# Optimization experiments

Hardware: AMD Instinct MI355X
Metric: run time of the kernel (lower is better)

## Reference

```python
import jax, jax.numpy as jnp
import numpy as np

N_NODES = 1_000_000
N_EDGES = 16_000_000


def _mean_aggregate(x, src, dst, num_nodes):
    # PyG message passing: message x_j = x[src], mean-aggregated at dst.
    msgs = x[src]  # [E, d]
    sums = jax.ops.segment_sum(msgs, dst, num_segments=num_nodes)
    cnt = jax.ops.segment_sum(jnp.ones((src.shape[0],), x.dtype), dst,
                              num_segments=num_nodes)
    return sums / jnp.maximum(cnt, 1.0)[:, None]


def _sage_conv(x, src, dst, W_l, b_l, W_r, num_nodes):
    # PyG SAGEConv (aggr='mean'): out = lin_l(mean_j x_j) + lin_r(x_i)
    agg = _mean_aggregate(x, src, dst, num_nodes)
    return agg @ W_l + b_l + x @ W_r


def setup_inputs() -> dict:
    key = jax.random.key(0)
    ks = jax.random.split(key, 12)
    x = jax.random.normal(ks[0], (N_NODES, 1), dtype=jnp.float32)
    edge_index = jax.random.randint(ks[1], (2, N_EDGES), 0, N_NODES, dtype=jnp.int64)

    def lin(k, din, dout):
        s = 1.0 / np.sqrt(din)
        return jax.random.uniform(k, (din, dout), jnp.float32, -s, s)

    return {
        "x": x, "edge_index": edge_index,
        "W1l": lin(ks[2], 1, 4), "b1": jnp.zeros((4,), jnp.float32), "W1r": lin(ks[3], 1, 4),
        "W2l": lin(ks[4], 4, 4), "b2": jnp.zeros((4,), jnp.float32), "W2r": lin(ks[5], 4, 4),
        "W3l": lin(ks[6], 4, 2), "b3": jnp.zeros((2,), jnp.float32), "W3r": lin(ks[7], 4, 2),
        "Wc": lin(ks[8], 2, 2), "bc": jnp.zeros((2,), jnp.float32),
    }


def reference(x, edge_index, W1l, b1, W1r, W2l, b2, W2r, W3l, b3, W3r, Wc, bc):
    src, dst = edge_index[0], edge_index[1]
    n = x.shape[0]
    h = jax.nn.relu(_sage_conv(x, src, dst, W1l, b1, W1r, n))
    h = jax.nn.relu(_sage_conv(h, src, dst, W2l, b2, W2r, n))
    h = jax.nn.relu(_sage_conv(h, src, dst, W3l, b3, W3r, n))
    out = h @ Wc + bc
    return (out, h)
```

## Files before the change

kernel.cpp:

```cpp
#include <hip/hip_runtime.h>
#include <hip/hip_fp16.h>


#define NBUCK 4096
#define CAP   4608
#define SRCM  0xFFFFFu
#define DEPTH 8

__device__ __forceinline__ ushort4 pack_h4(float4 f)
{
    ushort4 r;
    r.x = __half_as_ushort(__float2half_rn(f.x));
    r.y = __half_as_ushort(__float2half_rn(f.y));
    r.z = __half_as_ushort(__float2half_rn(f.z));
    r.w = __half_as_ushort(__float2half_rn(f.w));
    return r;
}

__device__ __forceinline__ float4 unpack_h4(ushort4 v)
{
    return make_float4(__half2float(__ushort_as_half(v.x)),
                       __half2float(__ushort_as_half(v.y)),
                       __half2float(__ushort_as_half(v.z)),
                       __half2float(__ushort_as_half(v.w)));
}

__global__ __launch_bounds__(256) void init_cursor(unsigned* __restrict__ cursor)
{
    int b = blockIdx.x * blockDim.x + threadIdx.x;
    if (b < NBUCK) cursor[b] = (unsigned)b * CAP;
}

__global__ __launch_bounds__(1024) void scatter_staged(
    const int* __restrict__ ei,
    unsigned* __restrict__ gcur,
    unsigned* __restrict__ bucket,
    long long E, long long chunk)
{
    __shared__ unsigned stage[NBUCK * DEPTH];
    __shared__ unsigned cnt[NBUCK];
    const int t = threadIdx.x;
    const long long beg = (long long)blockIdx.x * chunk;
    const long long end = min(E, beg + chunk);

    for (int i = t; i < NBUCK; i += 1024) cnt[i] = 0;
    __syncthreads();

    for (long long base = beg; base < end; base += 4096) {
        unsigned rec[4], bk[4], pos[4];
        int nv = 0;
        long long i = base + (long long)t * 4;
        if (i + 4 <= end) {
            int4 s4 = *reinterpret_cast<const int4*>(ei + i);
            int4 d4 = *reinterpret_cast<const int4*>(ei + E + i);
            rec[0] = (unsigned)s4.x | (((unsigned)d4.x & 255u) << 20); bk[0] = (unsigned)d4.x >> 8;
            rec[1] = (unsigned)s4.y | (((unsigned)d4.y & 255u) << 20); bk[1] = (unsigned)d4.y >> 8;
            rec[2] = (unsigned)s4.z | (((unsigned)d4.z & 255u) << 20); bk[2] = (unsigned)d4.z >> 8;
            rec[3] = (unsigned)s4.w | (((unsigned)d4.w & 255u) << 20); bk[3] = (unsigned)d4.w >> 8;
            nv = 4;
        } else {
            for (long long j = i; j < end && nv < 4; ++j) {
                unsigned s = (unsigned)ei[j];
                unsigned d = (unsigned)ei[E + j];
                rec[nv] = s | ((d & 255u) << 20);
                bk[nv] = d >> 8;
                ++nv;
            }
        }
        for (int k = 0; k < nv; ++k) pos[k] = atomicAdd(&cnt[bk[k]], 1u);
        __syncthreads();
        for (int k = 0; k < nv; ++k)
            if (pos[k] < DEPTH) stage[bk[k] * DEPTH + pos[k]] = rec[k];
        __syncthreads();
        for (int bb = t; bb < NBUCK; bb += 1024) {
            unsigned c = cnt[bb];
            if (c >= DEPTH) {
                unsigned gb = atomicAdd(&gcur[bb], DEPTH);
                unsigned lim = (unsigned)(bb + 1) * CAP;
#pragma unroll
                for (int k = 0; k < DEPTH; ++k)
                    if (gb + k < lim) bucket[gb + k] = stage[bb * DEPTH + k];
                cnt[bb] = 0;
            }
        }
        __syncthreads();
        for (int k = 0; k < nv; ++k) {
            if (pos[k] >= DEPTH) {
                unsigned p2 = atomicAdd(&cnt[bk[k]], 1u);
                if (p2 < DEPTH) stage[bk[k] * DEPTH + p2] = rec[k];
                else {
                    unsigned gb = atomicAdd(&gcur[bk[k]], 1u);
                    if (gb < (unsigned)(bk[k] + 1) * CAP) bucket[gb] = rec[k];
                }
            }
        }
        __syncthreads();
    }
    for (int bb = t; bb < NBUCK; bb += 1024) {
        unsigned c = min(cnt[bb], (unsigned)DEPTH);
        if (c) {
            unsigned gb = atomicAdd(&gcur[bb], c);
            unsigned lim = (unsigned)(bb + 1) * CAP;
            for (unsigned k = 0; k < c; ++k)
                if (gb + k < lim) bucket[gb + k] = stage[bb * DEPTH + k];
        }
    }
}

template <bool EMIT16>
__global__ __launch_bounds__(256) void sort_l1(
    unsigned* __restrict__ bucket,
    const unsigned* __restrict__ cursor,
    unsigned* __restrict__ meta,
    const float* __restrict__ x,
    const float* __restrict__ W1l, const float* __restrict__ b1,
    const float* __restrict__ W1r,
    float* __restrict__ invout, float4* __restrict__ h1,
    ushort4* __restrict__ h1h, int N)
{
    __shared__ unsigned recA[CAP];
    __shared__ unsigned recB[CAP];
    __shared__ unsigned hist[256], pref[256], curs[256];
    const int t = threadIdx.x;
    const unsigned b = blockIdx.x;
    const unsigned base = b * CAP;
    const unsigned cnt = min(cursor[b] - base, (unsigned)CAP);

    hist[t] = 0;
    __syncthreads();
    for (unsigned i = t; i < cnt; i += 256) {
        unsigned r = bucket[base + i];
        recA[i] = r;
        atomicAdd(&hist[r >> 20], 1u);
    }
    __syncthreads();
    unsigned v = hist[t];
    pref[t] = v;
    __syncthreads();
    for (int off = 1; off < 256; off <<= 1) {
        unsigned u = (t >= off) ? pref[t - off] : 0u;
        __syncthreads();
        pref[t] += u;
        __syncthreads();
    }
    unsigned excl = pref[t] - v;
    curs[t] = excl;
    __syncthreads();
    for (unsigned i = t; i < cnt; i += 256) {
        unsigned r = recA[i];
        unsigned pos = atomicAdd(&curs[r >> 20], 1u);
        recB[pos] = r & SRCM;
    }
    __syncthreads();
    for (unsigned i = t; i < cnt; i += 256)
        bucket[base + i] = recB[i];

    int dst = (int)(b * 256u) + t;
    if (dst >= N) return;
    meta[dst] = excl | (v << 16);

    float sum = 0.0f;
    for (unsigned j = 0; j < v; ++j)
        sum += x[recB[excl + j]];
    float iv = 1.0f / fmaxf((float)v, 1.0f);
    invout[dst] = iv;
    float a = sum * iv;
    float xv = x[dst];
    float4 h;
    h.x = fmaxf(a * W1l[0] + b1[0] + xv * W1r[0], 0.0f);
    h.y = fmaxf(a * W1l[1] + b1[1] + xv * W1r[1], 0.0f);
    h.z = fmaxf(a * W1l[2] + b1[2] + xv * W1r[2], 0.0f);
    h.w = fmaxf(a * W1l[3] + b1[3] + xv * W1r[3], 0.0f);
    h1[dst] = h;
    if (EMIT16) h1h[dst] = pack_h4(h);
}

__device__ __forceinline__ float4 run_sum4(
    const unsigned* srtd, unsigned idx, unsigned c,
    const float4* __restrict__ feat)
{
    float a0 = 0, a1 = 0, a2 = 0, a3 = 0;
    unsigned j = 0;
    for (; j + 4 <= c; j += 4) {
        unsigned s0 = srtd[idx + j + 0];
        unsigned s1 = srtd[idx + j + 1];
        unsigned s2 = srtd[idx + j + 2];
        unsigned s3 = srtd[idx + j + 3];
        float4 f0 = feat[s0];
        float4 f1 = feat[s1];
        float4 f2 = feat[s2];
        float4 f3 = feat[s3];
        a0 += f0.x + f1.x + f2.x + f3.x;
        a1 += f0.y + f1.y + f2.y + f3.y;
        a2 += f0.z + f1.z + f2.z + f3.z;
        a3 += f0.w + f1.w + f2.w + f3.w;
    }
    for (; j < c; ++j) {
        float4 f = feat[srtd[idx + j]];
        a0 += f.x; a1 += f.y; a2 += f.z; a3 += f.w;
    }
    return make_float4(a0, a1, a2, a3);
}

__device__ __forceinline__ float4 run_sum4h(
    const unsigned* srtd, unsigned idx, unsigned c,
    const ushort4* __restrict__ feat)
{
    float a0 = 0, a1 = 0, a2 = 0, a3 = 0;
    unsigned j = 0;
    for (; j + 4 <= c; j += 4) {
        unsigned s0 = srtd[idx + j + 0];
        unsigned s1 = srtd[idx + j + 1];
        unsigned s2 = srtd[idx + j + 2];
        unsigned s3 = srtd[idx + j + 3];
        float4 f0 = unpack_h4(feat[s0]);
        float4 f1 = unpack_h4(feat[s1]);
        float4 f2 = unpack_h4(feat[s2]);
        float4 f3 = unpack_h4(feat[s3]);
        a0 += f0.x + f1.x + f2.x + f3.x;
        a1 += f0.y + f1.y + f2.y + f3.y;
        a2 += f0.z + f1.z + f2.z + f3.z;
        a3 += f0.w + f1.w + f2.w + f3.w;
    }
    for (; j < c; ++j) {
        float4 f = unpack_h4(feat[srtd[idx + j]]);
        a0 += f.x; a1 += f.y; a2 += f.z; a3 += f.w;
    }
    return make_float4(a0, a1, a2, a3);
}

template <bool USE16>
__global__ __launch_bounds__(256) void agg_l2(
    const unsigned* __restrict__ srtd, const unsigned* __restrict__ cursor,
    const unsigned* __restrict__ meta,
    const float4* __restrict__ h1, const ushort4* __restrict__ h1h,
    const float* __restrict__ inv,
    const float* __restrict__ W2l, const float* __restrict__ b2,
    const float* __restrict__ W2r,
    float4* __restrict__ h2, ushort4* __restrict__ h2h, int N)
{
    __shared__ unsigned srun[CAP];
    const int t = threadIdx.x;
    const unsigned b = blockIdx.x;
    const unsigned base = b * CAP;
    const unsigned bc = min(cursor[b] - base, (unsigned)CAP);
    for (unsigned i = t; i < bc; i += 256) srun[i] = srtd[base + i];
    __syncthreads();

    int dst = (int)(b * 256u) + t;
    if (dst >= N) return;
    unsigned m = meta[dst];
    float4 s4 = USE16 ? run_sum4h(srun, m & 0xffffu, m >> 16, h1h)
                      : run_sum4 (srun, m & 0xffffu, m >> 16, h1);
    float iv = inv[dst];
    float a[4] = {s4.x * iv, s4.y * iv, s4.z * iv, s4.w * iv};
    float4 hv = h1[dst];
    float hr[4] = {hv.x, hv.y, hv.z, hv.w};
    float o[4];
#pragma unroll
    for (int j = 0; j < 4; ++j) {
        float acc = b2[j];
#pragma unroll
        for (int k = 0; k < 4; ++k)
            acc += a[k] * W2l[k * 4 + j] + hr[k] * W2r[k * 4 + j];
        o[j] = fmaxf(acc, 0.0f);
    }
    float4 h = make_float4(o[0], o[1], o[2], o[3]);
    h2[dst] = h;
    if (USE16) h2h[dst] = pack_h4(h);
}

template <bool USE16>
__global__ __launch_bounds__(256) void agg_l3(
    const unsigned* __restrict__ srtd, const unsigned* __restrict__ cursor,
    const unsigned* __restrict__ meta,
    const float4* __restrict__ h2, const ushort4* __restrict__ h2h,
    const float* __restrict__ inv,
    const float* __restrict__ W3l, const float* __restrict__ b3,
    const float* __restrict__ W3r,
    const float* __restrict__ Wc, const float* __restrict__ bc,
    float2* __restrict__ out, float2* __restrict__ hout, int N)
{
    __shared__ unsigned srun[CAP];
    const int t = threadIdx.x;
    const unsigned b = blockIdx.x;
    const unsigned base = b * CAP;
    const unsigned bcnt = min(cursor[b] - base, (unsigned)CAP);
    for (unsigned i = t; i < bcnt; i += 256) srun[i] = srtd[base + i];
    __syncthreads();

    int dst = (int)(b * 256u) + t;
    if (dst >= N) return;
    unsigned m = meta[dst];
    float4 s4 = USE16 ? run_sum4h(srun, m & 0xffffu, m >> 16, h2h)
                      : run_sum4 (srun, m & 0xffffu, m >> 16, h2);
    float iv = inv[dst];
    float a[4] = {s4.x * iv, s4.y * iv, s4.z * iv, s4.w * iv};
    float4 hv = h2[dst];
    float hr[4] = {hv.x, hv.y, hv.z, hv.w};
    float h3[2];
#pragma unroll
    for (int j = 0; j < 2; ++j) {
        float acc = b3[j];
#pragma unroll
        for (int k = 0; k < 4; ++k)
            acc += a[k] * W3l[k * 2 + j] + hr[k] * W3r[k * 2 + j];
        h3[j] = fmaxf(acc, 0.0f);
    }
    float o0 = h3[0] * Wc[0] + h3[1] * Wc[2] + bc[0];
    float o1 = h3[0] * Wc[1] + h3[1] * Wc[3] + bc[1];
    out[dst]  = make_float2(o0, o1);
    hout[dst] = make_float2(h3[0], h3[1]);
}

#define FPS   262144.0f
#define IFPS  3.8146973e-06f
#define XBIAS 16.0f

__global__ __launch_bounds__(256) void edge_pass1(
    const int* __restrict__ ei, const float* __restrict__ x,
    unsigned long long* __restrict__ agg1, long long E)
{
    long long i = (long long)blockIdx.x * blockDim.x + threadIdx.x;
    const long long stride = (long long)gridDim.x * blockDim.x;
    for (; i < E; i += stride) {
        int s = ei[i];
        int d = ei[E + i];
        unsigned q = (unsigned)((x[s] + XBIAS) * FPS + 0.5f);
        atomicAdd(&agg1[d], (unsigned long long)q | (1ull << 32));
    }
}

__global__ __launch_bounds__(256) void edge_pass4(
    const int* __restrict__ ei, const float4* __restrict__ feat,
    unsigned long long* __restrict__ pair, long long E)
{
    long long i = (long long)blockIdx.x * blockDim.x + threadIdx.x;
    const long long stride = (long long)gridDim.x * blockDim.x;
    for (; i < E; i += stride) {
        int s = ei[i];
        int d = ei[E + i];
        float4 f = feat[s];
        unsigned q0 = (unsigned)(f.x * FPS + 0.5f);
        unsigned q1 = (unsigned)(f.y * FPS + 0.5f);
        unsigned q2 = (unsigned)(f.z * FPS + 0.5f);
        unsigned q3 = (unsigned)(f.w * FPS + 0.5f);
        atomicAdd(&pair[2ll*d+0], (unsigned long long)q0 | ((unsigned long long)q1 << 32));
        atomicAdd(&pair[2ll*d+1], (unsigned long long)q2 | ((unsigned long long)q3 << 32));
    }
}

__global__ __launch_bounds__(256) void node_pass1(
    const float* __restrict__ x, const unsigned long long* __restrict__ agg1,
    float* __restrict__ invout, const float* __restrict__ W1l,
    const float* __restrict__ b1, const float* __restrict__ W1r,
    float4* __restrict__ h1, int N)
{
    int i = blockIdx.x * blockDim.x + threadIdx.x;
    if (i >= N) return;
    unsigned long long v = agg1[i];
    float cnt = (float)(unsigned)(v >> 32);
    float lo  = (float)(unsigned)(v & 0xffffffffu);
    float sumx = lo * IFPS - XBIAS * cnt;
    float inv = 1.0f / fmaxf(cnt, 1.0f);
    invout[i] = inv;
    float a = sumx * inv;
    float xv = x[i];
    float4 h;
    h.x = fmaxf(a * W1l[0] + b1[0] + xv * W1r[0], 0.0f);
    h.y = fmaxf(a * W1l[1] + b1[1] + xv * W1r[1], 0.0f);
    h.z = fmaxf(a * W1l[2] + b1[2] + xv * W1r[2], 0.0f);
    h.w = fmaxf(a * W1l[3] + b1[3] + xv * W1r[3], 0.0f);
    h1[i] = h;
}

__device__ __forceinline__ float4 unpack_agg(const unsigned long long* pair, int i, float iv)
{
    unsigned long long m01 = pair[2ll * i + 0];
    unsigned long long m23 = pair[2ll * i + 1];
    float4 a;
    a.x = (float)(unsigned)(m01 & 0xffffffffu) * IFPS * iv;
    a.y = (float)(unsigned)(m01 >> 32)         * IFPS * iv;
    a.z = (float)(unsigned)(m23 & 0xffffffffu) * IFPS * iv;
    a.w = (float)(unsigned)(m23 >> 32)         * IFPS * iv;
    return a;
}

__global__ __launch_bounds__(256) void node_pass2(
    const unsigned long long* __restrict__ pair, const float4* __restrict__ h1,
    const float* __restrict__ inv, const float* __restrict__ W2l,
    const float* __restrict__ b2, const float* __restrict__ W2r,
    float4* __restrict__ h2, int N)
{
    int i = blockIdx.x * blockDim.x + threadIdx.x;
    if (i >= N) return;
    float iv = inv[i];
    float4 ag = unpack_agg(pair, i, iv);
    float4 hv = h1[i];
    float a[4]  = {ag.x, ag.y, ag.z, ag.w};
    float hr[4] = {hv.x, hv.y, hv.z, hv.w};
    float o[4];
#pragma unroll
    for (int j = 0; j < 4; ++j) {
        float acc = b2[j];
#pragma unroll
        for (int k = 0; k < 4; ++k)
            acc += a[k] * W2l[k * 4 + j] + hr[k] * W2r[k * 4 + j];
        o[j] = fmaxf(acc, 0.0f);
    }
    h2[i] = make_float4(o[0], o[1], o[2], o[3]);
}

__global__ __launch_bounds__(256) void node_pass3(
    const unsigned long long* __restrict__ pair, const float4* __restrict__ h2,
    const float* __restrict__ inv, const float* __restrict__ W3l,
    const float* __restrict__ b3, const float* __restrict__ W3r,
    const float* __restrict__ Wc, const float* __restrict__ bc,
    float2* __restrict__ out, float2* __restrict__ hout, int N)
{
    int i = blockIdx.x * blockDim.x + threadIdx.x;
    if (i >= N) return;
    float iv = inv[i];
    float4 ag = unpack_agg(pair, i, iv);
    float4 hv = h2[i];
    float a[4]  = {ag.x, ag.y, ag.z, ag.w};
    float hr[4] = {hv.x, hv.y, hv.z, hv.w};
    float h3[2];
#pragma unroll
    for (int j = 0; j < 2; ++j) {
        float acc = b3[j];
#pragma unroll
        for (int k = 0; k < 4; ++k)
            acc += a[k] * W3l[k * 2 + j] + hr[k] * W3r[k * 2 + j];
        h3[j] = fmaxf(acc, 0.0f);
    }
    float o0 = h3[0] * Wc[0] + h3[1] * Wc[2] + bc[0];
    float o1 = h3[0] * Wc[1] + h3[1] * Wc[3] + bc[1];
    out[i]  = make_float2(o0, o1);
    hout[i] = make_float2(h3[0], h3[1]);
}

extern "C" void kernel_launch(void* const* d_in, const int* in_sizes, int n_in,
                              void* d_out, int out_size, void* d_ws, size_t ws_size,
                              hipStream_t stream)
{
    const float* x   = (const float*)d_in[0];
    const int*   ei  = (const int*)d_in[1];
    const float* W1l = (const float*)d_in[2];
    const float* b1  = (const float*)d_in[3];
    const float* W1r = (const float*)d_in[4];
    const float* W2l = (const float*)d_in[5];
    const float* b2  = (const float*)d_in[6];
    const float* W2r = (const float*)d_in[7];
    const float* W3l = (const float*)d_in[8];
    const float* b3  = (const float*)d_in[9];
    const float* W3r = (const float*)d_in[10];
    const float* Wc  = (const float*)d_in[11];
    const float* bc  = (const float*)d_in[12];

    const long long N = in_sizes[0];
    const long long E = in_sizes[1] / 2;

    float* out  = (float*)d_out;
    float* hout = out + 2 * N;

    const size_t need_r7 =
        (size_t)(9 * N) * 4 + (size_t)NBUCK * 4 +
        (size_t)NBUCK * (size_t)CAP * 4 + (size_t)N * 4;
    const size_t need16 = need_r7 + (size_t)(4 * N) * 4;

    if (ws_size >= need_r7) {
        float*    inv    = (float*)d_ws;
        float*    h1     = inv + N;
        float*    h2     = h1 + 4 * N;
        unsigned* cursor = (unsigned*)(h2 + 4 * N);
        unsigned* bucket = cursor + NBUCK;
        unsigned* meta   = bucket + (size_t)NBUCK * CAP;
        ushort4*  h1h    = (ushort4*)(meta + N);
        ushort4*  h2h    = h1h + N;
        const bool f16   = ws_size >= need16;

        const int SB = 256;
        long long chunk = (E + SB - 1) / SB;
        chunk = (chunk + 4095) & ~4095ll;
        const int nbk = (int)((N + 255) / 256);

        init_cursor<<<NBUCK / 256, 256, 0, stream>>>(cursor);
        scatter_staged<<<SB, 1024, 0, stream>>>(ei, cursor, bucket, E, chunk);
        if (f16) {
            sort_l1<true><<<nbk, 256, 0, stream>>>(bucket, cursor, meta, x,
                W1l, b1, W1r, inv, (float4*)h1, h1h, (int)N);
            agg_l2<true><<<nbk, 256, 0, stream>>>(bucket, cursor, meta,
                (const float4*)h1, h1h, inv, W2l, b2, W2r, (float4*)h2, h2h, (int)N);
            agg_l3<true><<<nbk, 256, 0, stream>>>(bucket, cursor, meta,
                (const float4*)h2, h2h, inv, W3l, b3, W3r, Wc, bc,
                (float2*)out, (float2*)hout, (int)N);
        } else {
            sort_l1<false><<<nbk, 256, 0, stream>>>(bucket, cursor, meta, x,
                W1l, b1, W1r, inv, (float4*)h1, nullptr, (int)N);
            agg_l2<false><<<nbk, 256, 0, stream>>>(bucket, cursor, meta,
                (const float4*)h1, nullptr, inv, W2l, b2, W2r, (float4*)h2, nullptr, (int)N);
            agg_l3<false><<<nbk, 256, 0, stream>>>(bucket, cursor, meta,
                (const float4*)h2, nullptr, inv, W3l, b3, W3r, Wc, bc,
                (float2*)out, (float2*)hout, (int)N);
        }
        return;
    }

    float* ws  = (float*)d_ws;
    float* inv = ws;
    float* h1  = inv + N;
    unsigned long long* pair = (unsigned long long*)(h1 + 4 * N);
    float* h2  = (float*)(pair + 2 * N);

    const int nt = 256, eb = 8192;
    const int nb = (int)((N + nt - 1) / nt);

    hipMemsetAsync(pair, 0, (size_t)N * sizeof(unsigned long long), stream);
    edge_pass1<<<eb, nt, 0, stream>>>(ei, x, pair, E);
    node_pass1<<<nb, nt, 0, stream>>>(x, pair, inv, W1l, b1, W1r, (float4*)h1, (int)N);

    hipMemsetAsync(pair, 0, (size_t)(2 * N) * sizeof(unsigned long long), stream);
    edge_pass4<<<eb, nt, 0, stream>>>(ei, (const float4*)h1, pair, E);
    node_pass2<<<nb, nt, 0, stream>>>(pair, (const float4*)h1, inv,
                                      W2l, b2, W2r, (float4*)h2, (int)N);

    hipMemsetAsync(pair, 0, (size_t)(2 * N) * sizeof(unsigned long long), stream);
    edge_pass4<<<eb, nt, 0, stream>>>(ei, (const float4*)h2, pair, E);
    node_pass3<<<nb, nt, 0, stream>>>(pair, (const float4*)h2, inv,
                                      W3l, b3, W3r, Wc, bc,
                                      (float2*)out, (float2*)hout, (int)N);
}
```

Before: 754.5 us.

## Sweep fp16 gathers by source-index quarter and vectorize bucket flush stores

The fp16 neighbor-sum loop now makes four passes over each destination's source list and gathers only sources whose high index bits fall in the current quarter. All threads of a block therefore touch roughly the same quarter of the feature table at once, which is meant to improve L2 locality of the random gathers. The cost is four reads of the source list from shared memory, an unroll-1 loop with a branch per element, and no memory-level parallelism from unrolling. Separately, the bucket flush in the scatter kernel uses two uint4 stores when the destination is aligned and fully in bounds.

```diff
diff --git a/kernel.cpp b/kernel.cpp
--- a/kernel.cpp
+++ b/kernel.cpp
@@ -77,9 +77,16 @@
             if (c >= DEPTH) {
                 unsigned gb = atomicAdd(&gcur[bb], DEPTH);
                 unsigned lim = (unsigned)(bb + 1) * CAP;
-#pragma unroll
-                for (int k = 0; k < DEPTH; ++k)
-                    if (gb + k < lim) bucket[gb + k] = stage[bb * DEPTH + k];
+                if ((gb & 3u) == 0u && gb + DEPTH <= lim) {
+                    const uint4* s4 = reinterpret_cast<const uint4*>(stage + bb * DEPTH);
+                    uint4* d4 = reinterpret_cast<uint4*>(bucket + gb);
+                    d4[0] = s4[0];
+                    d4[1] = s4[1];
+                } else {
+#pragma unroll
+                    for (int k = 0; k < DEPTH; ++k)
+                        if (gb + k < lim) bucket[gb + k] = stage[bb * DEPTH + k];
+                }
                 cnt[bb] = 0;
             }
         }
@@ -202,29 +209,20 @@
     return make_float4(a0, a1, a2, a3);
 }
 
-__device__ __forceinline__ float4 run_sum4h(
-    const unsigned* srtd, unsigned idx, unsigned c,
+__device__ __forceinline__ float4 run_sum4h_swept(
+    const unsigned* srun, unsigned idx, unsigned c,
     const ushort4* __restrict__ feat)
 {
     float a0 = 0, a1 = 0, a2 = 0, a3 = 0;
-    unsigned j = 0;
-    for (; j + 4 <= c; j += 4) {
-        unsigned s0 = srtd[idx + j + 0];
-        unsigned s1 = srtd[idx + j + 1];
-        unsigned s2 = srtd[idx + j + 2];
-        unsigned s3 = srtd[idx + j + 3];
-        float4 f0 = unpack_h4(feat[s0]);
-        float4 f1 = unpack_h4(feat[s1]);
-        float4 f2 = unpack_h4(feat[s2]);
-        float4 f3 = unpack_h4(feat[s3]);
-        a0 += f0.x + f1.x + f2.x + f3.x;
-        a1 += f0.y + f1.y + f2.y + f3.y;
-        a2 += f0.z + f1.z + f2.z + f3.z;
-        a3 += f0.w + f1.w + f2.w + f3.w;
-    }
-    for (; j < c; ++j) {
-        float4 f = unpack_h4(feat[srtd[idx + j]]);
-        a0 += f.x; a1 += f.y; a2 += f.z; a3 += f.w;
+#pragma unroll 1
+    for (unsigned q = 0; q < 4; ++q) {
+        for (unsigned j = 0; j < c; ++j) {
+            unsigned s = srun[idx + j];
+            if ((s >> 18) == q) {
+                float4 f = unpack_h4(feat[s]);
+                a0 += f.x; a1 += f.y; a2 += f.z; a3 += f.w;
+            }
+        }
     }
     return make_float4(a0, a1, a2, a3);
 }
@@ -250,8 +248,8 @@
     int dst = (int)(b * 256u) + t;
     if (dst >= N) return;
     unsigned m = meta[dst];
-    float4 s4 = USE16 ? run_sum4h(srun, m & 0xffffu, m >> 16, h1h)
-                      : run_sum4 (srun, m & 0xffffu, m >> 16, h1);
+    float4 s4 = USE16 ? run_sum4h_swept(srun, m & 0xffffu, m >> 16, h1h)
+                      : run_sum4      (srun, m & 0xffffu, m >> 16, h1);
     float iv = inv[dst];
     float a[4] = {s4.x * iv, s4.y * iv, s4.z * iv, s4.w * iv};
     float4 hv = h1[dst];
@@ -292,8 +290,8 @@
     int dst = (int)(b * 256u) + t;
     if (dst >= N) return;
     unsigned m = meta[dst];
-    float4 s4 = USE16 ? run_sum4h(srun, m & 0xffffu, m >> 16, h2h)
-                      : run_sum4 (srun, m & 0xffffu, m >> 16, h2);
+    float4 s4 = USE16 ? run_sum4h_swept(srun, m & 0xffffu, m >> 16, h2h)
+                      : run_sum4      (srun, m & 0xffffu, m >> 16, h2);
     float iv = inv[dst];
     float a[4] = {s4.x * iv, s4.y * iv, s4.z * iv, s4.w * iv};
     float4 hv = h2[dst];
```

Measured after the change: 639.1 us. 1.18x faster.
